# Kernel optimization log

Hardware: AMD Instinct MI355X
Metric: run time of the kernel (lower is better)

Reference implementation:

```python
import jax, jax.numpy as jnp
import numpy as np

B, S, D = 4, 2048, 1024
H, HD = 16, 64
WINDOW = 128


def setup_inputs() -> dict:
    key = jax.random.key(0)
    ks = jax.random.split(key, 8)
    scale = 1.0 / np.sqrt(D)
    return {
        "hidden_states": jax.random.normal(ks[0], (B, S, D), dtype=jnp.float32),
        "attention_mask": jnp.zeros((B, 1, 1, S), dtype=jnp.float32),
        "Wq": jax.random.normal(ks[1], (D, D), dtype=jnp.float32) * scale,
        "bq": jnp.zeros((D,), dtype=jnp.float32),
        "Wk": jax.random.normal(ks[2], (D, D), dtype=jnp.float32) * scale,
        "bk": jnp.zeros((D,), dtype=jnp.float32),
        "Wv": jax.random.normal(ks[3], (D, D), dtype=jnp.float32) * scale,
        "bv": jnp.zeros((D,), dtype=jnp.float32),
    }


def _proj(x, W, b):
    # [b t D] -> [b h t d]
    p = x @ W.T + b
    return p.reshape(x.shape[0], x.shape[1], H, HD).transpose(0, 2, 1, 3)


def reference(hidden_states, attention_mask, Wq, bq, Wk, bk, Wv, bv):
    q = _proj(hidden_states, Wq, bq)  # [b h t d]
    k = _proj(hidden_states, Wk, bk)
    v = _proj(hidden_states, Wv, bv)

    scores = jnp.einsum("bhtd,bhsd->bhts", q, k) / np.sqrt(HD)  # [b h t s]
    pos = jnp.arange(S)
    i, j = pos[:, None], pos[None, :]
    # causal (j <= i) AND sliding window (i - j <= w)
    allowed = (j <= i) & ((i - j) <= WINDOW)  # [t s]
    scores = jnp.where(allowed[None, None], scores, -jnp.inf)
    scores = scores + attention_mask  # additive padding mask [b,1,1,s]
    probs = jax.nn.softmax(scores, axis=-1)  # dropout identity in eval
    ctx = jnp.einsum("bhts,bhsd->bhtd", probs, v)
    return ctx.transpose(0, 2, 1, 3).reshape(B, S, D)
```

## Files before the change

### kernel.cpp

```cpp
#include <hip/hip_runtime.h>
#include <cstdint>

#define BDIM 4
#define SEQ 2048
#define DMODEL 1024
#define NH 16
#define HDIM 64

typedef __attribute__((ext_vector_type(8))) short bf16x8;
typedef __attribute__((ext_vector_type(4))) float f32x4;
typedef __attribute__((ext_vector_type(4))) int i32x4;
typedef __attribute__((ext_vector_type(4))) unsigned short u16x4;

#define MFMA16(a, b, c) __builtin_amdgcn_mfma_f32_16x16x32_bf16(a, b, c, 0, 0, 0)

__device__ __forceinline__ unsigned short f2bf(float x) {
    unsigned int u = __float_as_uint(x);
    unsigned int r = (u + 0x7FFFu + ((u >> 16) & 1u)) >> 16;
    return (unsigned short)r;
}

__device__ __forceinline__ void gload16(const void* g, void* l) {
    __builtin_amdgcn_global_load_lds(
        (const __attribute__((address_space(1))) unsigned int*)g,
        (__attribute__((address_space(3))) unsigned int*)l, 16, 0, 0);
}

__global__ __launch_bounds__(256) void k_cvt_x(const float* __restrict__ src,
                                               unsigned short* __restrict__ dst) {
    int i = blockIdx.x * 256 + threadIdx.x;
    float4 v = ((const float4*)src)[i];
    u16x4 o = {f2bf(v.x), f2bf(v.y), f2bf(v.z), f2bf(v.w)};
    ((u16x4*)dst)[i] = o;
}

__global__ __launch_bounds__(256) void k_cvt_w(const float* __restrict__ wq,
                                               const float* __restrict__ wk,
                                               const float* __restrict__ wv,
                                               unsigned short* __restrict__ dst) {
    int i = blockIdx.x * 256 + threadIdx.x;
    int e = i << 2;
    int which = e >> 20;
    int off = e & 0xFFFFF;
    const float* s = which == 0 ? wq : (which == 1 ? wk : wv);
    float4 v = *(const float4*)(s + off);
    u16x4 o = {f2bf(v.x), f2bf(v.y), f2bf(v.z), f2bf(v.w)};
    ((u16x4*)dst)[i] = o;
}

__global__ __launch_bounds__(256) void k_qkv(const unsigned short* __restrict__ X,
                                             const unsigned short* __restrict__ W,
                                             const float* __restrict__ bq,
                                             const float* __restrict__ bk,
                                             const float* __restrict__ bv,
                                             unsigned short* __restrict__ Qo,
                                             unsigned short* __restrict__ Ko,
                                             unsigned short* __restrict__ Vt) {
    __shared__ unsigned short ldsA[128 * 32];
    __shared__ unsigned short ldsB[128 * 32];
    const int tid = threadIdx.x;
    const int lane = tid & 63, wid = tid >> 6;
    const int wm = wid >> 1, wn = wid & 1;
    const int l15 = lane & 15, g = lane >> 4;
    const int m0 = blockIdx.y * 128, n0 = blockIdx.x * 128;

    f32x4 acc[4][4];
#pragma unroll
    for (int i = 0; i < 4; ++i)
#pragma unroll
        for (int j = 0; j < 4; ++j) acc[i][j] = (f32x4){0.f, 0.f, 0.f, 0.f};

    for (int kt = 0; kt < 32; ++kt) {
        const int k0 = kt << 5;
        __syncthreads();
#pragma unroll
        for (int it = 0; it < 2; ++it) {
            const int c = it * 256 + tid;
            const int row = c >> 2, sl = c & 3;
            gload16(X + (size_t)(m0 + row) * DMODEL + k0 + sl * 8, (char*)ldsA + c * 16);
            gload16(W + (size_t)(n0 + row) * DMODEL + k0 + sl * 8, (char*)ldsB + c * 16);
        }
        __syncthreads();
        bf16x8 a[4], b[4];
#pragma unroll
        for (int f = 0; f < 4; ++f) {
            a[f] = *(const bf16x8*)((const char*)ldsA + (wm * 64 + f * 16 + l15) * 64 + g * 16);
            b[f] = *(const bf16x8*)((const char*)ldsB + (wn * 64 + f * 16 + l15) * 64 + g * 16);
        }
#pragma unroll
        for (int fm = 0; fm < 4; ++fm)
#pragma unroll
            for (int fn = 0; fn < 4; ++fn) acc[fm][fn] = MFMA16(a[fm], b[fn], acc[fm][fn]);
    }

#pragma unroll
    for (int fn = 0; fn < 4; ++fn) {
        const int col = n0 + wn * 64 + fn * 16 + l15;
        const int proj = col >> 10, rem = col & 1023;
        const int h = rem >> 6, hd = rem & 63;
        const float* bp = proj == 0 ? bq : (proj == 1 ? bk : bv);
        const float bias = bp[rem];
        if (proj == 2) {
#pragma unroll
            for (int fm = 0; fm < 4; ++fm) {
                const int mb = m0 + wm * 64 + fm * 16 + g * 4;
                const int bb = mb >> 11, s = mb & 2047;
                u16x4 ov = {f2bf(acc[fm][fn][0] + bias), f2bf(acc[fm][fn][1] + bias),
                            f2bf(acc[fm][fn][2] + bias), f2bf(acc[fm][fn][3] + bias)};
                *(u16x4*)(Vt + (size_t)((bb * NH + h) * HDIM + hd) * SEQ + s) = ov;
            }
        } else {
            const float scl = (proj == 0) ? 0.125f : 1.0f;
            unsigned short* dst = proj == 0 ? Qo : Ko;
#pragma unroll
            for (int fm = 0; fm < 4; ++fm) {
#pragma unroll
                for (int r = 0; r < 4; ++r) {
                    const int m = m0 + wm * 64 + fm * 16 + g * 4 + r;
                    const int bb = m >> 11, s = m & 2047;
                    dst[(size_t)((bb * NH + h) * SEQ + s) * HDIM + hd] =
                        f2bf((acc[fm][fn][r] + bias) * scl);
                }
            }
        }
    }
}

__global__ __launch_bounds__(256) void k_attn(const unsigned short* __restrict__ Qg,
                                              const unsigned short* __restrict__ Kg,
                                              const unsigned short* __restrict__ Vtg,
                                              const float* __restrict__ amask,
                                              float* __restrict__ out) {
    __shared__ unsigned short kl[224 * 64];
    __shared__ unsigned short vl[64 * 224];
    __shared__ unsigned short pl[4 * 16 * 160];
    const int bid0 = blockIdx.x;
    const int bid = (bid0 & 7) * 256 + (bid0 >> 3);
    const int bh = bid >> 5, qb = bid & 31;
    const int b = bh >> 4, h = bh & 15;
    const int q0 = qb << 6;
    const int kstart = q0 - 144;
    const int tid = threadIdx.x, lane = tid & 63, w = tid >> 6;
    const int l15 = lane & 15, g = lane >> 4;

#pragma unroll
    for (int it = 0; it < 7; ++it) {
        const int c = it * 256 + tid;
        {
            const int row = c >> 3, sl = c & 7;
            const int key = kstart + row;
            i32x4 v = {0, 0, 0, 0};
            if ((unsigned)key < (unsigned)SEQ)
                v = *(const i32x4*)(Kg + (size_t)(bh * SEQ + key) * HDIM + sl * 8);
            *(i32x4*)((char*)kl + ((row * 128 + sl * 16) ^ ((row & 7) << 4))) = v;
        }
        {
            const int row = c / 28, sl = c - row * 28;
            const int key0 = kstart + sl * 8;
            i32x4 v = {0, 0, 0, 0};
            if ((unsigned)key0 < (unsigned)SEQ)
                v = *(const i32x4*)(Vtg + (size_t)(bh * HDIM + row) * SEQ + key0);
            *(i32x4*)((char*)vl + ((row * 448 + sl * 16) ^ ((row & 7) << 4))) = v;
        }
    }
    const int iq = q0 + w * 16 + l15;
    const bf16x8 qf0 = *(const bf16x8*)(Qg + (size_t)(bh * SEQ + iq) * HDIM + g * 8);
    const bf16x8 qf1 = *(const bf16x8*)(Qg + (size_t)(bh * SEQ + iq) * HDIM + 32 + g * 8);
    __syncthreads();

    char* pbase = (char*)pl + w * 5120;
    const int swq = (l15 & 7) << 4;
    float s[40];

    __builtin_amdgcn_s_setprio(1);
#pragma unroll
    for (int t = 0; t < 5; ++t) {
        const int tloc = w * 16 + t * 32;
        bf16x8 kf[2][2];
#pragma unroll
        for (int m = 0; m < 2; ++m) {
            const int row = tloc + m * 16 + l15;
            const int swz = (row & 7) << 4;
            kf[m][0] = *(const bf16x8*)((const char*)kl + ((row * 128 + g * 16) ^ swz));
            kf[m][1] = *(const bf16x8*)((const char*)kl + ((row * 128 + 64 + g * 16) ^ swz));
        }
        f32x4 sa0 = {0.f, 0.f, 0.f, 0.f}, sa1 = {0.f, 0.f, 0.f, 0.f};
        sa0 = MFMA16(kf[0][0], qf0, sa0);
        sa0 = MFMA16(kf[0][1], qf1, sa0);
        sa1 = MFMA16(kf[1][0], qf0, sa1);
        sa1 = MFMA16(kf[1][1], qf1, sa1);
#pragma unroll
        for (int f = 0; f < 2; ++f) {
            const int jb = kstart + tloc + f * 16 + g * 4;
            float4 m4 = {0.f, 0.f, 0.f, 0.f};
            if ((unsigned)jb < (unsigned)SEQ) m4 = *(const float4*)(amask + b * SEQ + jb);
            const float mvv[4] = {m4.x, m4.y, m4.z, m4.w};
#pragma unroll
            for (int r = 0; r < 4; ++r) {
                const int jg = jb + r;
                const float sc = (f == 0 ? sa0[r] : sa1[r]) + mvv[r];
                const bool ok = (jg >= 0) && (jg <= iq) && (iq - jg <= 128);
                s[t * 8 + f * 4 + r] = ok ? sc : -3.0e38f;
            }
        }
    }
    __builtin_amdgcn_s_setprio(0);

    float tr[20];
#pragma unroll
    for (int i = 0; i < 20; ++i) tr[i] = fmaxf(s[i], s[i + 20]);
#pragma unroll
    for (int i = 0; i < 10; ++i) tr[i] = fmaxf(tr[i], tr[i + 10]);
#pragma unroll
    for (int i = 0; i < 5; ++i) tr[i] = fmaxf(tr[i], tr[i + 5]);
    float m = fmaxf(fmaxf(tr[0], tr[1]), fmaxf(tr[2], fmaxf(tr[3], tr[4])));
    m = fmaxf(m, __shfl_xor(m, 16));
    m = fmaxf(m, __shfl_xor(m, 32));

    float ls0 = 0.f, ls1 = 0.f, ls2 = 0.f, ls3 = 0.f;
#pragma unroll
    for (int i = 0; i < 40; i += 4) {
        float p0 = exp2f((s[i + 0] - m) * 1.44269504f);
        float p1 = exp2f((s[i + 1] - m) * 1.44269504f);
        float p2 = exp2f((s[i + 2] - m) * 1.44269504f);
        float p3 = exp2f((s[i + 3] - m) * 1.44269504f);
        s[i + 0] = p0; s[i + 1] = p1; s[i + 2] = p2; s[i + 3] = p3;
        ls0 += p0; ls1 += p1; ls2 += p2; ls3 += p3;
    }
    float l = (ls0 + ls1) + (ls2 + ls3);
    l += __shfl_xor(l, 16);
    l += __shfl_xor(l, 32);

#pragma unroll
    for (int t = 0; t < 5; ++t) {
#pragma unroll
        for (int f = 0; f < 2; ++f) {
            u16x4 pu = {f2bf(s[t * 8 + f * 4 + 0]), f2bf(s[t * 8 + f * 4 + 1]),
                        f2bf(s[t * 8 + f * 4 + 2]), f2bf(s[t * 8 + f * 4 + 3])};
            *(u16x4*)(pbase + ((l15 * 320 + t * 64 + f * 32 + g * 8) ^ swq)) = pu;
        }
    }
    asm volatile("s_waitcnt lgkmcnt(0)" ::: "memory");
    __builtin_amdgcn_sched_barrier(0);

    f32x4 acc[4];
#pragma unroll
    for (int i = 0; i < 4; ++i) acc[i] = (f32x4){0.f, 0.f, 0.f, 0.f};
    __builtin_amdgcn_s_setprio(1);
#pragma unroll
    for (int t = 0; t < 5; ++t) {
        const int tloc = w * 16 + t * 32;
        const bf16x8 pf = *(const bf16x8*)(pbase + ((l15 * 320 + t * 64 + g * 16) ^ swq));
#pragma unroll
        for (int fn = 0; fn < 4; ++fn) {
            const int vrow = fn * 16 + l15;
            const bf16x8 vf = *(const bf16x8*)((const char*)vl +
                ((vrow * 448 + tloc * 2 + g * 16) ^ ((vrow & 7) << 4)));
            acc[fn] = MFMA16(pf, vf, acc[fn]);
        }
    }
    __builtin_amdgcn_s_setprio(0);

    float linv[4];
#pragma unroll
    for (int r = 0; r < 4; ++r) linv[r] = 1.0f / __shfl(l, g * 4 + r);
#pragma unroll
    for (int fn = 0; fn < 4; ++fn) {
#pragma unroll
        for (int r = 0; r < 4; ++r) {
            const int qrow = q0 + w * 16 + g * 4 + r;
            out[(size_t)(b * SEQ + qrow) * DMODEL + h * HDIM + fn * 16 + l15] =
                acc[fn][r] * linv[r];
        }
    }
}

extern "C" void kernel_launch(void* const* d_in, const int* in_sizes, int n_in,
                              void* d_out, int out_size, void* d_ws, size_t ws_size,
                              hipStream_t stream) {
    const float* hs = (const float*)d_in[0];
    const float* amask = (const float*)d_in[1];
    const float* wq = (const float*)d_in[2];
    const float* bq = (const float*)d_in[3];
    const float* wk = (const float*)d_in[4];
    const float* bk = (const float*)d_in[5];
    const float* wv = (const float*)d_in[6];
    const float* bv = (const float*)d_in[7];
    float* out = (float*)d_out;

    char* p = (char*)d_ws;
    unsigned short* Xbf = (unsigned short*)p;
    unsigned short* Wbf = (unsigned short*)(p + 16777216);
    unsigned short* Vtb = (unsigned short*)(p + 16777216 + 6291456);
    unsigned short* Qb = Vtb + 8388608;
    unsigned short* Kb = Qb + 8388608;

    k_cvt_x<<<8192, 256, 0, stream>>>(hs, Xbf);
    k_cvt_w<<<3072, 256, 0, stream>>>(wq, wk, wv, Wbf);
    k_qkv<<<dim3(24, 64), 256, 0, stream>>>(Xbf, Wbf, bq, bk, bv, Qb, Kb, Vtb);
    k_attn<<<2048, 256, 0, stream>>>(Qb, Kb, Vtb, amask, out);
}
```

Measured before the change: 131.5 us.

## Deepen QKV GEMM K-tile to 64 with XOR-swizzled LDS and unified epilogue

The QKV projection GEMM now stages a 64-wide K slice per iteration instead of 32. That halves the number of barrier pairs and doubles the MFMA work done between syncs. LDS rows are XOR-swizzled so that the wider 128-byte rows avoid bank conflicts on fragment reads, and a waves_per_eu hint is added. The epilogue is merged into a single strided scalar-store path, which gives up the vectorized u16x4 stores for V and may cost some store efficiency.

```diff
diff --git a/kernel.cpp b/kernel.cpp
--- a/kernel.cpp
+++ b/kernel.cpp
@@ -48,16 +48,17 @@
     ((u16x4*)dst)[i] = o;
 }
 
-__global__ __launch_bounds__(256) void k_qkv(const unsigned short* __restrict__ X,
-                                             const unsigned short* __restrict__ W,
-                                             const float* __restrict__ bq,
-                                             const float* __restrict__ bk,
-                                             const float* __restrict__ bv,
-                                             unsigned short* __restrict__ Qo,
-                                             unsigned short* __restrict__ Ko,
-                                             unsigned short* __restrict__ Vt) {
-    __shared__ unsigned short ldsA[128 * 32];
-    __shared__ unsigned short ldsB[128 * 32];
+__global__ __launch_bounds__(256) __attribute__((amdgpu_waves_per_eu(4)))
+void k_qkv(const unsigned short* __restrict__ X,
+           const unsigned short* __restrict__ W,
+           const float* __restrict__ bq,
+           const float* __restrict__ bk,
+           const float* __restrict__ bv,
+           unsigned short* __restrict__ Qo,
+           unsigned short* __restrict__ Ko,
+           unsigned short* __restrict__ Vt) {
+    __shared__ unsigned short ldsA[128 * 64];
+    __shared__ unsigned short ldsB[128 * 64];
     const int tid = threadIdx.x;
     const int lane = tid & 63, wid = tid >> 6;
     const int wm = wid >> 1, wn = wid & 1;
@@ -70,58 +71,56 @@
 #pragma unroll
         for (int j = 0; j < 4; ++j) acc[i][j] = (f32x4){0.f, 0.f, 0.f, 0.f};
 
-    for (int kt = 0; kt < 32; ++kt) {
-        const int k0 = kt << 5;
+    for (int kt = 0; kt < 16; ++kt) {
+        const int k0 = kt << 6;
         __syncthreads();
 #pragma unroll
-        for (int it = 0; it < 2; ++it) {
+        for (int it = 0; it < 4; ++it) {
             const int c = it * 256 + tid;
-            const int row = c >> 2, sl = c & 3;
-            gload16(X + (size_t)(m0 + row) * DMODEL + k0 + sl * 8, (char*)ldsA + c * 16);
-            gload16(W + (size_t)(n0 + row) * DMODEL + k0 + sl * 8, (char*)ldsB + c * 16);
+            const int row = c >> 3, sl = c & 7;
+            const int slx = sl ^ (row & 7);
+            gload16(X + (size_t)(m0 + row) * DMODEL + k0 + slx * 8, (char*)ldsA + c * 16);
+            gload16(W + (size_t)(n0 + row) * DMODEL + k0 + slx * 8, (char*)ldsB + c * 16);
         }
         __syncthreads();
-        bf16x8 a[4], b[4];
-#pragma unroll
-        for (int f = 0; f < 4; ++f) {
-            a[f] = *(const bf16x8*)((const char*)ldsA + (wm * 64 + f * 16 + l15) * 64 + g * 16);
-            b[f] = *(const bf16x8*)((const char*)ldsB + (wn * 64 + f * 16 + l15) * 64 + g * 16);
-        }
-#pragma unroll
-        for (int fm = 0; fm < 4; ++fm)
-#pragma unroll
-            for (int fn = 0; fn < 4; ++fn) acc[fm][fn] = MFMA16(a[fm], b[fn], acc[fm][fn]);
-    }
-
+#pragma unroll
+        for (int kk = 0; kk < 2; ++kk) {
+            bf16x8 a[4], b[4];
+#pragma unroll
+            for (int f = 0; f < 4; ++f) {
+                const int ra = wm * 64 + f * 16 + l15;
+                a[f] = *(const bf16x8*)((const char*)ldsA +
+                        ((ra * 128 + kk * 64 + g * 16) ^ ((ra & 7) << 4)));
+                const int rb = wn * 64 + f * 16 + l15;
+                b[f] = *(const bf16x8*)((const char*)ldsB +
+                        ((rb * 128 + kk * 64 + g * 16) ^ ((rb & 7) << 4)));
+            }
+#pragma unroll
+            for (int fm = 0; fm < 4; ++fm)
+#pragma unroll
+                for (int fn = 0; fn < 4; ++fn) acc[fm][fn] = MFMA16(a[fm], b[fn], acc[fm][fn]);
+        }
+    }
+
+    const int bb = m0 >> 11;
+    const int sbase = (m0 & 2047) + wm * 64 + g * 4;
 #pragma unroll
     for (int fn = 0; fn < 4; ++fn) {
         const int col = n0 + wn * 64 + fn * 16 + l15;
         const int proj = col >> 10, rem = col & 1023;
         const int h = rem >> 6, hd = rem & 63;
-        const float* bp = proj == 0 ? bq : (proj == 1 ? bk : bv);
-        const float bias = bp[rem];
-        if (proj == 2) {
-#pragma unroll
-            for (int fm = 0; fm < 4; ++fm) {
-                const int mb = m0 + wm * 64 + fm * 16 + g * 4;
-                const int bb = mb >> 11, s = mb & 2047;
-                u16x4 ov = {f2bf(acc[fm][fn][0] + bias), f2bf(acc[fm][fn][1] + bias),
-                            f2bf(acc[fm][fn][2] + bias), f2bf(acc[fm][fn][3] + bias)};
-                *(u16x4*)(Vt + (size_t)((bb * NH + h) * HDIM + hd) * SEQ + s) = ov;
-            }
-        } else {
-            const float scl = (proj == 0) ? 0.125f : 1.0f;
-            unsigned short* dst = proj == 0 ? Qo : Ko;
-#pragma unroll
-            for (int fm = 0; fm < 4; ++fm) {
-#pragma unroll
-                for (int r = 0; r < 4; ++r) {
-                    const int m = m0 + wm * 64 + fm * 16 + g * 4 + r;
-                    const int bb = m >> 11, s = m & 2047;
-                    dst[(size_t)((bb * NH + h) * SEQ + s) * HDIM + hd] =
-                        f2bf((acc[fm][fn][r] + bias) * scl);
-                }
-            }
+        const float bias = (proj == 0 ? bq : proj == 1 ? bk : bv)[rem];
+        const float scl = (proj == 0) ? 0.125f : 1.0f;
+        unsigned short* dstp = (proj == 0 ? Qo : proj == 1 ? Ko : Vt) +
+                               (size_t)(bb * NH + h) * (SEQ * HDIM) +
+                               (proj == 2 ? (size_t)hd * SEQ : (size_t)hd);
+        const int stride = (proj == 2) ? 1 : HDIM;
+#pragma unroll
+        for (int fm = 0; fm < 4; ++fm) {
+            const int s0 = sbase + fm * 16;
+#pragma unroll
+            for (int r = 0; r < 4; ++r)
+                dstp[(size_t)(s0 + r) * stride] = f2bf((acc[fm][fn][r] + bias) * scl);
         }
     }
 }
```

New measurement: 138.2 us. 1.05x slower.
